# Kernel tuning notes

Measured on AMD Instinct MI355X. Metric: run time of the kernel, lower is better.

## Reference

```python
import jax, jax.numpy as jnp
import numpy as np

N_ITER = 50  # entmax_bisect default


def _p(t, alpha):
    # (clamp(t, min=0)) ** (1/(alpha-1))
    return jnp.maximum(t, 0.0) ** (1.0 / (alpha - 1.0))


def entmax_bisect(X, alpha):
    """alpha-entmax over last axis via bisection (Peters et al.), matching
    entmax.entmax_bisect with n_iter=50, ensure_sum_one=True."""
    d = X.shape[-1]
    Xa = X * (alpha - 1.0)
    max_val = jnp.max(Xa, axis=-1, keepdims=True)
    tau_lo = max_val - 1.0                                  # _gp_inv(1)
    tau_hi = max_val - (1.0 / d) ** (alpha - 1.0)           # _gp_inv(1/d)
    f_lo = jnp.sum(_p(Xa - tau_lo, alpha), -1, keepdims=True) - 1.0

    def body(i, carry):
        tau_lo, dm, tau_m = carry
        dm = dm * 0.5
        tau_m = tau_lo + dm
        f_m = jnp.sum(_p(Xa - tau_m, alpha), -1, keepdims=True) - 1.0
        tau_lo = jnp.where(f_m * f_lo >= 0.0, tau_m, tau_lo)
        return (tau_lo, dm, tau_m)

    tau_lo, dm, tau_m = jax.lax.fori_loop(
        0, N_ITER, body, (tau_lo, tau_hi - tau_lo, tau_lo))
    p = _p(Xa - tau_m, alpha)
    return p / jnp.sum(p, -1, keepdims=True)


def setup_inputs() -> dict:
    key = jax.random.key(0)
    ks = jax.random.split(key, 9)
    B, C, E, H = 2, 256, 512, 8
    s = 0.05
    inp = {
        "x":  jax.random.normal(ks[0], (B, C, E), jnp.float32),
        "Wq": jax.random.normal(ks[1], (E, E * H), jnp.float32) * s,
        "bq": jax.random.normal(ks[2], (E * H,), jnp.float32) * s,
        "Wk": jax.random.normal(ks[3], (E, E * H), jnp.float32) * s,
        "bk": jax.random.normal(ks[4], (E * H,), jnp.float32) * s,
        "Wv": jax.random.normal(ks[5], (E, E * H), jnp.float32) * s,
        "bv": jax.random.normal(ks[6], (E * H,), jnp.float32) * s,
        "Wu": jax.random.normal(ks[7], (E * H, E), jnp.float32) * s,
        "bu": jax.random.normal(ks[8], (E,), jnp.float32) * s,
        "alpha": jnp.asarray(1.5, jnp.float32),
    }
    return inp


def reference(x, Wq, bq, Wk, bk, Wv, bv, Wu, bu, alpha):
    b, c, e = x.shape
    h = Wq.shape[1] // e
    q = (x @ Wq + bq).reshape(b, c, h, e)
    k = (x @ Wk + bk).reshape(b, c, h, e)
    v = (x @ Wv + bv).reshape(b, c, h, e)
    # q.transpose(-2,-1) @ k : contracts over heads -> (b, c, e, e)
    dot = jnp.einsum('bchi,bchj->bcij', q, k) / (e ** 0.5)
    p = entmax_bisect(dot, alpha)                    # (b, c, e, e)
    # (p @ v^T).transpose(-2,-1) -> (b, c, h, e) -> reshape (b, c, h*e)
    res = jnp.einsum('bcij,bchj->bchi', p, v).reshape(b, c, h * e)
    return res @ Wu + bu
```

## Files before the change

kernel.cpp:

```cpp
#include <hip/hip_runtime.h>
#include <hip/hip_bf16.h>
#include <stdint.h>

typedef float f32x2 __attribute__((ext_vector_type(2)));

__device__ __forceinline__ f32x2 mk2(float a, float b) { f32x2 r; r.x = a; r.y = b; return r; }
__device__ __forceinline__ f32x2 bc2(float a) { f32x2 r; r.x = a; r.y = a; return r; }
__device__ __forceinline__ f32x2 max2(f32x2 a, f32x2 b) {
#if __has_builtin(__builtin_elementwise_max)
    return __builtin_elementwise_max(a, b);
#else
    return mk2(fmaxf(a.x, b.x), fmaxf(a.y, b.y));
#endif
}
__device__ __forceinline__ f32x2 min2(f32x2 a, f32x2 b) {
#if __has_builtin(__builtin_elementwise_min)
    return __builtin_elementwise_min(a, b);
#else
    return mk2(fminf(a.x, b.x), fminf(a.y, b.y));
#endif
}

typedef __fp16 half2v __attribute__((ext_vector_type(2)));
typedef __fp16 f16x8v __attribute__((ext_vector_type(8)));
typedef float f32x4v __attribute__((ext_vector_type(4)));

__device__ __forceinline__ half2v u2h(uint32_t u) {
    union { uint32_t u; half2v h; } c; c.u = u; return c.h;
}
__device__ __forceinline__ uint32_t pk(float lo, float hi) {
    union { uint32_t u; half2v h; } c;
    c.h = __builtin_amdgcn_cvt_pkrtz(lo, hi);
    return c.u;
}
__device__ __forceinline__ f16x8v u4h8(uint4 u) {
    union { uint4 u; f16x8v h; } c; c.u = u; return c.h;
}
#if __has_builtin(__builtin_amdgcn_fdot2)
__device__ __forceinline__ float dot2(uint32_t a, uint32_t b, float c) {
    return __builtin_amdgcn_fdot2(u2h(a), u2h(b), c, false);
}
#else
__device__ __forceinline__ float dot2(uint32_t a, uint32_t b, float c) {
    float d;
    asm("v_dot2_f32_f16 %0, %1, %2, %3" : "=v"(d) : "v"(a), "v"(b), "v"(c));
    return d;
}
#endif

template <int CTRL>
__device__ __forceinline__ float dppmov(float v) {
    return __int_as_float(__builtin_amdgcn_update_dpp(
        0, __float_as_int(v), CTRL, 0xF, 0xF, true));
}
__device__ __forceinline__ float grp_sum16(float v) {
    v += dppmov<0xB1>(v);
    v += dppmov<0x4E>(v);
    v += dppmov<0x124>(v);
    v += dppmov<0x128>(v);
    return v;
}
__device__ __forceinline__ float grp_max16(float v) {
    v = fmaxf(v, dppmov<0xB1>(v));
    v = fmaxf(v, dppmov<0x4E>(v));
    v = fmaxf(v, dppmov<0x124>(v));
    v = fmaxf(v, dppmov<0x128>(v));
    return v;
}

__global__ __launch_bounds__(256) void gemm_mfma(
    const float* __restrict__ A, int lda,
    const float* __restrict__ B, int ldb,
    float* __restrict__ C, int ldc,
    int M, int N, int kc, const float* __restrict__ bias)
{
    __shared__ uint32_t AhU[64 * 28];
    __shared__ uint32_t BhU[64 * 28];
    const int tid = threadIdx.x;
    const int bm = blockIdx.y * 64;
    const int bn = blockIdx.x * 64;
    const int k0 = blockIdx.z * kc;
    C += (size_t)blockIdx.z * M * N;

    const int lane = tid & 63;
    const int w = tid >> 6;
    const int lr = lane & 15;
    const int lg = lane >> 4;

    f32x4v acc[4];
#pragma unroll
    for (int nt = 0; nt < 4; ++nt) acc[nt] = (f32x4v)(0.0f);

    const int sar = tid >> 2;
    const int sak = (tid & 3) * 8;
    const int sbn = (tid & 15) * 4;
    const int sbk = (tid >> 4) * 2;

    for (int kt = k0; kt < k0 + kc; kt += 32) {
        float4 a0 = *(const float4*)&A[(size_t)(bm + sar) * lda + kt + sak];
        float4 a1 = *(const float4*)&A[(size_t)(bm + sar) * lda + kt + sak + 4];
        float4 b0 = *(const float4*)&B[(size_t)(kt + sbk) * ldb + bn + sbn];
        float4 b1 = *(const float4*)&B[(size_t)(kt + sbk + 1) * ldb + bn + sbn];
        __syncthreads();
        *(uint4*)&AhU[sar * 28 + (tid & 3) * 4] =
            make_uint4(pk(a0.x, a0.y), pk(a0.z, a0.w),
                       pk(a1.x, a1.y), pk(a1.z, a1.w));
        BhU[(sbn + 0) * 28 + (tid >> 4)] = pk(b0.x, b1.x);
        BhU[(sbn + 1) * 28 + (tid >> 4)] = pk(b0.y, b1.y);
        BhU[(sbn + 2) * 28 + (tid >> 4)] = pk(b0.z, b1.z);
        BhU[(sbn + 3) * 28 + (tid >> 4)] = pk(b0.w, b1.w);
        __syncthreads();

        f16x8v af = u4h8(*(const uint4*)&AhU[(16 * w + lr) * 28 + lg * 4]);
#pragma unroll
        for (int nt = 0; nt < 4; ++nt) {
            f16x8v bf = u4h8(*(const uint4*)&BhU[(nt * 16 + lr) * 28 + lg * 4]);
            acc[nt] = __builtin_amdgcn_mfma_f32_16x16x32_f16(af, bf, acc[nt], 0, 0, 0);
        }
    }

#pragma unroll
    for (int nt = 0; nt < 4; ++nt) {
        const int col = bn + nt * 16 + lr;
        const float badd = bias ? bias[col] : 0.0f;
#pragma unroll
        for (int reg = 0; reg < 4; ++reg) {
            const int row = bm + 16 * w + 4 * lg + reg;
            C[(size_t)row * ldc + col] = acc[nt][reg] + badd;
        }
    }
}

#define QROWS 128
#define NSOLVE 2
#define NBISECT 3
#define NNEWTON 6

__global__ __launch_bounds__(256, 4) void attn_entmax(
    const float* __restrict__ qg, const float* __restrict__ kg,
    const float* __restrict__ vg, float* resg,
    const float* __restrict__ alpha_p)
{
    __shared__ uint32_t ks16[4 * 512];
    __shared__ uint32_t vs16[8 * 256];
    const int t = blockIdx.x >> 2;
    const int base = (blockIdx.x & 3) * QROWS;
    const int tid = threadIdx.x;

    const float alpha = alpha_p[0];
    const float expo = 1.0f / (alpha - 1.0f);
    const bool fast = (expo == 2.0f);
    const float scl = (alpha - 1.0f) * 0.04419417382415922f;
    const float hispan = powf(1.0f / 512.0f, alpha - 1.0f);

    const float qmul = fast ? 4.0f * scl : scl;
    const float TGT  = fast ? 16.0f : 1.0f;
    const float loO  = fast ? 4.0f : 1.0f;
    const float hiO  = (fast ? 4.0f : 1.0f) * hispan;

    {
        const float4* k4g = (const float4*)(kg + (size_t)t * 4096);
        const float4* v4g = (const float4*)(vg + (size_t)t * 4096);
#pragma unroll
        for (int a0 = 0; a0 < 2; ++a0) {
            int idx = tid + 256 * a0;
            int h2 = idx >> 7, j4 = idx & 127;
            float4 g0 = k4g[(2 * h2) * 128 + j4];
            float4 g1 = k4g[(2 * h2 + 1) * 128 + j4];
            uint4 p4 = make_uint4(pk(g0.x, g1.x), pk(g0.y, g1.y),
                                  pk(g0.z, g1.z), pk(g0.w, g1.w));
            *(uint4*)&ks16[h2 * 512 + j4 * 4] = p4;
        }
#pragma unroll
        for (int a0 = 0; a0 < 4; ++a0) {
            int f = tid + 256 * a0;
            int h = f >> 7, j4 = f & 127;
            float4 g = v4g[h * 128 + j4];
            uint2 p2 = make_uint2(pk(g.x, g.y), pk(g.z, g.w));
            *(uint2*)&vs16[h * 256 + j4 * 2] = p2;
        }
    }
    __syncthreads();

    const int lane = tid & 63;
    const int w = tid >> 6;
    const int sub = lane >> 4;
    const int lx = lane & 15;

    const f32x2 zero2 = bc2(0.0f);
    const f32x2 one2  = bc2(1.0f);
    const f32x2 big2  = bc2(1e30f);

    const float* qt = qg + (size_t)t * 4096 + base;
    const int r0 = w * 4 + sub;

    float qv[8];
#pragma unroll
    for (int h = 0; h < 8; ++h) qv[h] = qt[h * 512 + r0];

    for (int it = 0; it < QROWS / 16; ++it) {
        const int il = it * 16 + r0;

        uint32_t qp[4];
#pragma unroll
        for (int h2 = 0; h2 < 4; ++h2)
            qp[h2] = pk(qv[2 * h2] * qmul, qv[2 * h2 + 1] * qmul);

        f32x2 x2[16];
        f32x2 mv = bc2(-1e30f), sv = zero2;
#pragma unroll 2
        for (int u = 0; u < 8; ++u) {
            float a0 = 0, a1 = 0, a2 = 0, a3 = 0;
#pragma unroll
            for (int h2 = 0; h2 < 4; ++h2) {
                uint4 kk = *(const uint4*)&ks16[h2 * 512 + lx * 4 + 64 * u];
                uint32_t qh = qp[h2];
                a0 = dot2(kk.x, qh, a0);
                a1 = dot2(kk.y, qh, a1);
                a2 = dot2(kk.z, qh, a2);
                a3 = dot2(kk.w, qh, a3);
            }
            f32x2 A = mk2(a0, a1), B = mk2(a2, a3);
            x2[2 * u] = A;
            x2[2 * u + 1] = B;
            mv = max2(mv, max2(A, B));
            sv = sv + A + B;
        }

        if (it + 1 < QROWS / 16) {
#pragma unroll
            for (int h = 0; h < 8; ++h) qv[h] = qt[h * 512 + il + 16];
        }

        float m = grp_max16(fmaxf(mv.x, mv.y));
        const float tlo = m - loO;
        const float thi = m - hiO;

        float tau;
        if (fast) {
            float s1a = grp_sum16(sv.x + sv.y);
            tau = fminf(fmaxf(s1a * (1.0f / 512.0f), tlo), thi);
#pragma unroll
            for (int itr = 0; itr < NSOLVE; ++itr) {
                f32x2 tau2 = bc2(tau);
                f32x2 s1A = zero2, s1B = zero2;
                f32x2 s2A = zero2, s2B = zero2;
                f32x2 cA = zero2, cB = zero2;
#pragma unroll
                for (int j = 0; j < 16; j += 2) {
                    f32x2 rA = x2[j] - tau2;
                    f32x2 rB = x2[j + 1] - tau2;
                    f32x2 rpA = max2(rA, zero2);
                    f32x2 rpB = max2(rB, zero2);
                    s1A = s1A + rpA;
                    s1B = s1B + rpB;
                    s2A = rpA * rpA + s2A;
                    s2B = rpB * rpB + s2B;
                    cA = cA + min2(rpA * big2, one2);
                    cB = cB + min2(rpB * big2, one2);
                }
                f32x2 s1v = s1A + s1B, s2v = s2A + s2B, cv = cA + cB;
                float s1 = grp_sum16(s1v.x + s1v.y);
                float s2 = grp_sum16(s2v.x + s2v.y);
                float nf = grp_sum16(cv.x + cv.y);
                float disc = fmaxf(fmaf(s1, s1, -nf * (s2 - TGT)), 0.0f);
                tau += (s1 - sqrtf(disc)) / fmaxf(nf, 1.0f);
                tau = fminf(fmaxf(tau, tlo), thi);
            }
        } else {
            tau = tlo;
            float dm = loO - hiO;
#pragma unroll
            for (int bi = 0; bi < NBISECT; ++bi) {
                dm *= 0.5f;
                float tm = tau + dm;
                float f = 0.0f;
#pragma unroll
                for (int j = 0; j < 16; ++j) {
                    f += __powf(fmaxf(x2[j].x - tm, 0.0f), expo);
                    f += __powf(fmaxf(x2[j].y - tm, 0.0f), expo);
                }
                f = grp_sum16(f);
                if (f >= TGT) tau = tm;
            }
#pragma unroll
            for (int ni = 0; ni < NNEWTON; ++ni) {
                float f = 0.0f, g = 0.0f;
#pragma unroll
                for (int j = 0; j < 16; ++j) {
                    float r0s = fmaxf(x2[j].x - tau, 0.0f);
                    float rp0 = __powf(r0s, expo - 1.0f);
                    g += rp0; f += rp0 * r0s;
                    float r1s = fmaxf(x2[j].y - tau, 0.0f);
                    float rp1 = __powf(r1s, expo - 1.0f);
                    g += rp1; f += rp1 * r1s;
                }
                f = grp_sum16(f);
                g = grp_sum16(g);
                tau += (f - TGT) / fmaxf(expo * g, 1e-30f);
                tau = fminf(fmaxf(tau, tlo), thi);
            }
        }

        float S;
        if (fast) {
            f32x2 tau2 = bc2(tau);
            f32x2 SA = zero2, SB = zero2;
#pragma unroll
            for (int j = 0; j < 16; j += 2) {
                f32x2 rA = max2(x2[j] - tau2, zero2);
                f32x2 rB = max2(x2[j + 1] - tau2, zero2);
                f32x2 pA = rA * rA;
                f32x2 pB = rB * rB;
                SA = SA + pA;
                SB = SB + pB;
                x2[j].x = __uint_as_float(pk(pA.x, pA.y));
                x2[j + 1].x = __uint_as_float(pk(pB.x, pB.y));
            }
            f32x2 Sv = SA + SB;
            S = Sv.x + Sv.y;
        } else {
            float s0 = 0.0f;
#pragma unroll
            for (int j = 0; j < 16; ++j) {
                float p0 = __powf(fmaxf(x2[j].x - tau, 0.0f), expo);
                float p1 = __powf(fmaxf(x2[j].y - tau, 0.0f), expo);
                s0 += p0 + p1;
                x2[j].x = __uint_as_float(pk(p0, p1));
            }
            S = s0;
        }
        S = grp_sum16(S);
        const float invS = 1.0f / S;

#pragma unroll
        for (int h = 0; h < 8; ++h) {
            float aA = 0.0f, aB = 0.0f;
#pragma unroll 2
            for (int u = 0; u < 8; ++u) {
                uint2 vv = *(const uint2*)&vs16[h * 256 + lx * 2 + 32 * u];
                aA = dot2(__float_as_uint(x2[2 * u].x), vv.x, aA);
                aB = dot2(__float_as_uint(x2[2 * u + 1].x), vv.y, aB);
            }
            float a = grp_sum16(aA + aB) * invS;
            if (lx == h) resg[(size_t)t * 4096 + h * 512 + base + il] = a;
        }
    }
}

__global__ __launch_bounds__(256) void reduce_bias(
    const float* __restrict__ part, const float* __restrict__ bu,
    float* __restrict__ out, int MN, int S)
{
    int i = blockIdx.x * 256 + threadIdx.x;
    if (i >= MN) return;
    float a = bu[i & 511];
#pragma unroll
    for (int s = 0; s < 8; ++s) a += part[(size_t)s * MN + i];
    out[i] = a;
}

extern "C" void kernel_launch(void* const* d_in, const int* in_sizes, int n_in,
                              void* d_out, int out_size, void* d_ws, size_t ws_size,
                              hipStream_t stream)
{
    const float* x  = (const float*)d_in[0];
    const float* Wq = (const float*)d_in[1];
    const float* bq = (const float*)d_in[2];
    const float* Wk = (const float*)d_in[3];
    const float* bk = (const float*)d_in[4];
    const float* Wv = (const float*)d_in[5];
    const float* bv = (const float*)d_in[6];
    const float* Wu = (const float*)d_in[7];
    const float* bu = (const float*)d_in[8];
    const float* al = (const float*)d_in[9];
    float* out = (float*)d_out;
    float* ws = (float*)d_ws;

    float* q = ws;
    float* k = ws + 2097152;
    float* v = ws + 2 * 2097152;
    float* res = q;
    float* part = k;

    dim3 blk(256);

    dim3 g1(4096 / 64, 512 / 64, 1);
    gemm_mfma<<<g1, blk, 0, stream>>>(x, 512, Wq, 4096, q, 4096, 512, 4096, 512, bq);
    gemm_mfma<<<g1, blk, 0, stream>>>(x, 512, Wk, 4096, k, 4096, 512, 4096, 512, bk);
    gemm_mfma<<<g1, blk, 0, stream>>>(x, 512, Wv, 4096, v, 4096, 512, 4096, 512, bv);

    attn_entmax<<<dim3(2048), blk, 0, stream>>>(q, k, v, res, al);

    dim3 g3(512 / 64, 512 / 64, 8);
    gemm_mfma<<<g3, blk, 0, stream>>>(res, 4096, Wu, 512, part, 512, 512, 512, 512, nullptr);
    reduce_bias<<<dim3(262144 / 256), blk, 0, stream>>>(part, bu, out, 262144, 8);
}
```

Before: 232.2 us.

## Double-buffer GEMM tiles, merge QKV launches, cheaper second entmax solve step

The GEMM gets double-buffered shared memory with register prefetch of the next K tile, which removes one barrier per iteration and overlaps global loads with MFMA work. The three Q/K/V projection GEMMs are merged into one launch that indexes by blockIdx.z, saving launch overhead and filling the GPU better. In the alpha=1.5 entmax path, the second quadratic-root solve becomes a plain Newton step that drops the count accumulation and the sqrt. The Newton step may converge slightly less exactly than the quadratic solve, and the doubled LDS use may reduce occupancy.

```diff
diff --git a/kernel.cpp b/kernel.cpp
--- a/kernel.cpp
+++ b/kernel.cpp
@@ -68,20 +68,15 @@
     return v;
 }
 
-__global__ __launch_bounds__(256) void gemm_mfma(
+__device__ __forceinline__ void gemm_mfma_body(
     const float* __restrict__ A, int lda,
     const float* __restrict__ B, int ldb,
     float* __restrict__ C, int ldc,
-    int M, int N, int kc, const float* __restrict__ bias)
-{
-    __shared__ uint32_t AhU[64 * 28];
-    __shared__ uint32_t BhU[64 * 28];
+    int kc, int k0, int bm, int bn,
+    const float* __restrict__ bias,
+    uint32_t* AhU, uint32_t* BhU)
+{
     const int tid = threadIdx.x;
-    const int bm = blockIdx.y * 64;
-    const int bn = blockIdx.x * 64;
-    const int k0 = blockIdx.z * kc;
-    C += (size_t)blockIdx.z * M * N;
-
     const int lane = tid & 63;
     const int w = tid >> 6;
     const int lr = lane & 15;
@@ -96,25 +91,37 @@
     const int sbn = (tid & 15) * 4;
     const int sbk = (tid >> 4) * 2;
 
-    for (int kt = k0; kt < k0 + kc; kt += 32) {
-        float4 a0 = *(const float4*)&A[(size_t)(bm + sar) * lda + kt + sak];
-        float4 a1 = *(const float4*)&A[(size_t)(bm + sar) * lda + kt + sak + 4];
-        float4 b0 = *(const float4*)&B[(size_t)(kt + sbk) * ldb + bn + sbn];
-        float4 b1 = *(const float4*)&B[(size_t)(kt + sbk + 1) * ldb + bn + sbn];
-        __syncthreads();
-        *(uint4*)&AhU[sar * 28 + (tid & 3) * 4] =
+    const int nk = kc >> 5;
+
+    float4 a0 = *(const float4*)&A[(size_t)(bm + sar) * lda + k0 + sak];
+    float4 a1 = *(const float4*)&A[(size_t)(bm + sar) * lda + k0 + sak + 4];
+    float4 b0 = *(const float4*)&B[(size_t)(k0 + sbk) * ldb + bn + sbn];
+    float4 b1 = *(const float4*)&B[(size_t)(k0 + sbk + 1) * ldb + bn + sbn];
+
+    for (int ki = 0; ki < nk; ++ki) {
+        uint32_t* Ab = AhU + (ki & 1) * (64 * 28);
+        uint32_t* Bb = BhU + (ki & 1) * (64 * 28);
+        *(uint4*)&Ab[sar * 28 + (tid & 3) * 4] =
             make_uint4(pk(a0.x, a0.y), pk(a0.z, a0.w),
                        pk(a1.x, a1.y), pk(a1.z, a1.w));
-        BhU[(sbn + 0) * 28 + (tid >> 4)] = pk(b0.x, b1.x);
-        BhU[(sbn + 1) * 28 + (tid >> 4)] = pk(b0.y, b1.y);
-        BhU[(sbn + 2) * 28 + (tid >> 4)] = pk(b0.z, b1.z);
-        BhU[(sbn + 3) * 28 + (tid >> 4)] = pk(b0.w, b1.w);
+        Bb[(sbn + 0) * 28 + (tid >> 4)] = pk(b0.x, b1.x);
+        Bb[(sbn + 1) * 28 + (tid >> 4)] = pk(b0.y, b1.y);
+        Bb[(sbn + 2) * 28 + (tid >> 4)] = pk(b0.z, b1.z);
+        Bb[(sbn + 3) * 28 + (tid >> 4)] = pk(b0.w, b1.w);
         __syncthreads();
 
-        f16x8v af = u4h8(*(const uint4*)&AhU[(16 * w + lr) * 28 + lg * 4]);
+        if (ki + 1 < nk) {
+            const int kt = k0 + (ki + 1) * 32;
+            a0 = *(const float4*)&A[(size_t)(bm + sar) * lda + kt + sak];
+            a1 = *(const float4*)&A[(size_t)(bm + sar) * lda + kt + sak + 4];
+            b0 = *(const float4*)&B[(size_t)(kt + sbk) * ldb + bn + sbn];
+            b1 = *(const float4*)&B[(size_t)(kt + sbk + 1) * ldb + bn + sbn];
+        }
+
+        f16x8v af = u4h8(*(const uint4*)&Ab[(16 * w + lr) * 28 + lg * 4]);
 #pragma unroll
         for (int nt = 0; nt < 4; ++nt) {
-            f16x8v bf = u4h8(*(const uint4*)&BhU[(nt * 16 + lr) * 28 + lg * 4]);
+            f16x8v bf = u4h8(*(const uint4*)&Bb[(nt * 16 + lr) * 28 + lg * 4]);
             acc[nt] = __builtin_amdgcn_mfma_f32_16x16x32_f16(af, bf, acc[nt], 0, 0, 0);
         }
     }
@@ -131,8 +138,33 @@
     }
 }
 
+__global__ __launch_bounds__(256) void gemm_qkv(
+    const float* __restrict__ x,
+    const float* __restrict__ Wq, const float* __restrict__ bq, float* q,
+    const float* __restrict__ Wk, const float* __restrict__ bk, float* k,
+    const float* __restrict__ Wv, const float* __restrict__ bv, float* v)
+{
+    __shared__ uint32_t AhU[2 * 64 * 28];
+    __shared__ uint32_t BhU[2 * 64 * 28];
+    const float* B = Wq; const float* bias = bq; float* C = q;
+    if (blockIdx.z == 1) { B = Wk; bias = bk; C = k; }
+    if (blockIdx.z == 2) { B = Wv; bias = bv; C = v; }
+    gemm_mfma_body(x, 512, B, 4096, C, 4096, 512, 0,
+                   blockIdx.y * 64, blockIdx.x * 64, bias, AhU, BhU);
+}
+
+__global__ __launch_bounds__(256) void gemm_out(
+    const float* __restrict__ A, const float* __restrict__ Wu,
+    float* __restrict__ part)
+{
+    __shared__ uint32_t AhU[2 * 64 * 28];
+    __shared__ uint32_t BhU[2 * 64 * 28];
+    float* C = part + (size_t)blockIdx.z * 512 * 512;
+    gemm_mfma_body(A, 4096, Wu, 512, C, 512, 512, blockIdx.z * 512,
+                   blockIdx.y * 64, blockIdx.x * 64, nullptr, AhU, BhU);
+}
+
 #define QROWS 128
-#define NSOLVE 2
 #define NBISECT 3
 #define NNEWTON 6
 
@@ -240,18 +272,16 @@
         if (fast) {
             float s1a = grp_sum16(sv.x + sv.y);
             tau = fminf(fmaxf(s1a * (1.0f / 512.0f), tlo), thi);
-#pragma unroll
-            for (int itr = 0; itr < NSOLVE; ++itr) {
+
+            {
                 f32x2 tau2 = bc2(tau);
                 f32x2 s1A = zero2, s1B = zero2;
                 f32x2 s2A = zero2, s2B = zero2;
                 f32x2 cA = zero2, cB = zero2;
 #pragma unroll
                 for (int j = 0; j < 16; j += 2) {
-                    f32x2 rA = x2[j] - tau2;
-                    f32x2 rB = x2[j + 1] - tau2;
-                    f32x2 rpA = max2(rA, zero2);
-                    f32x2 rpB = max2(rB, zero2);
+                    f32x2 rpA = max2(x2[j] - tau2, zero2);
+                    f32x2 rpB = max2(x2[j + 1] - tau2, zero2);
                     s1A = s1A + rpA;
                     s1B = s1B + rpB;
                     s2A = rpA * rpA + s2A;
@@ -267,6 +297,25 @@
                 tau += (s1 - sqrtf(disc)) / fmaxf(nf, 1.0f);
                 tau = fminf(fmaxf(tau, tlo), thi);
             }
+            {
+                f32x2 tau2 = bc2(tau);
+                f32x2 s1A = zero2, s1B = zero2;
+                f32x2 s2A = zero2, s2B = zero2;
+#pragma unroll
+                for (int j = 0; j < 16; j += 2) {
+                    f32x2 rpA = max2(x2[j] - tau2, zero2);
+                    f32x2 rpB = max2(x2[j + 1] - tau2, zero2);
+                    s1A = s1A + rpA;
+                    s1B = s1B + rpB;
+                    s2A = rpA * rpA + s2A;
+                    s2B = rpB * rpB + s2B;
+                }
+                f32x2 s1v = s1A + s1B, s2v = s2A + s2B;
+                float s1 = grp_sum16(s1v.x + s1v.y);
+                float s2 = grp_sum16(s2v.x + s2v.y);
+                tau += (s2 - TGT) / fmaxf(2.0f * s1, 1e-20f);
+                tau = fminf(fmaxf(tau, tlo), thi);
+            }
         } else {
             tau = tlo;
             float dm = loO - hiO;
@@ -385,14 +434,11 @@
 
     dim3 blk(256);
 
-    dim3 g1(4096 / 64, 512 / 64, 1);
-    gemm_mfma<<<g1, blk, 0, stream>>>(x, 512, Wq, 4096, q, 4096, 512, 4096, 512, bq);
-    gemm_mfma<<<g1, blk, 0, stream>>>(x, 512, Wk, 4096, k, 4096, 512, 4096, 512, bk);
-    gemm_mfma<<<g1, blk, 0, stream>>>(x, 512, Wv, 4096, v, 4096, 512, 4096, 512, bv);
+    gemm_qkv<<<dim3(4096 / 64, 512 / 64, 3), blk, 0, stream>>>(
+        x, Wq, bq, q, Wk, bk, k, Wv, bv, v);
 
     attn_entmax<<<dim3(2048), blk, 0, stream>>>(q, k, v, res, al);
 
-    dim3 g3(512 / 64, 512 / 64, 8);
-    gemm_mfma<<<g3, blk, 0, stream>>>(res, 4096, Wu, 512, part, 512, 512, 512, 512, nullptr);
+    gemm_out<<<dim3(512 / 64, 512 / 64, 8), blk, 0, stream>>>(res, Wu, part);
     reduce_bias<<<dim3(262144 / 256), blk, 0, stream>>>(part, bu, out, 262144, 8);
 }
```

After: 202.9 us. 12.6% less time.
